# Kernel optimization log

Hardware: AMD Instinct MI355X
Metric: run time of the kernel (lower is better)

The kernel has to match this reference:

```python
import jax, jax.numpy as jnp
import numpy as np

B, N, DI, DS, DP, DM, S = 64, 4096, 64, 64, 64, 128, 7
NUM_ITER = 3
EPS_ATTN = 1e-8
LN_EPS = 1e-5


def setup_inputs() -> dict:
    key = jax.random.key(0)
    ks = jax.random.split(key, 12)
    rn = lambda k, shp, sc=1.0: (jax.random.normal(k, shp, jnp.float32) * sc)
    return {
        "x": rn(ks[0], (B, N, DI)),
        "ln_inp_g": jnp.ones((DI,), jnp.float32),
        "ln_inp_b": jnp.zeros((DI,), jnp.float32),
        "ln_slot_g": jnp.ones((DS,), jnp.float32),
        "ln_slot_b": jnp.zeros((DS,), jnp.float32),
        "slots_init": rn(ks[1], (1, S, DS)),
        "Wk": rn(ks[2], (DI, DP), 1.0 / np.sqrt(DI)),
        "Wv": rn(ks[3], (DI, DP), 1.0 / np.sqrt(DI)),
        "Wq": rn(ks[4], (DS, DP), 1.0 / np.sqrt(DS)),
        "gru_wih": rn(ks[5], (3 * DS, DP), 1.0 / np.sqrt(DS)),
        "gru_whh": rn(ks[6], (3 * DS, DS), 1.0 / np.sqrt(DS)),
        "gru_bih": jnp.zeros((3 * DS,), jnp.float32),
        "gru_bhh": jnp.zeros((3 * DS,), jnp.float32),
        "mlp_w1": rn(ks[7], (DS, DM), 1.0 / np.sqrt(DS)),
        "mlp_b1": jnp.zeros((DM,), jnp.float32),
        "mlp_w2": rn(ks[8], (DM, DS), 1.0 / np.sqrt(DM)),
        "mlp_b2": jnp.zeros((DS,), jnp.float32),
    }


def _layernorm(x, g, b):
    m = jnp.mean(x, axis=-1, keepdims=True)
    v = jnp.mean(jnp.square(x - m), axis=-1, keepdims=True)
    return (x - m) * jax.lax.rsqrt(v + LN_EPS) * g + b


def _gru_cell(u, h, wih, whh, bih, bhh):
    # PyTorch GRUCell semantics
    gi = u @ wih.T + bih  # [*, 3*DS]
    gh = h @ whh.T + bhh
    ir, iz, inn = jnp.split(gi, 3, axis=-1)
    hr, hz, hn = jnp.split(gh, 3, axis=-1)
    r = jax.nn.sigmoid(ir + hr)
    z = jax.nn.sigmoid(iz + hz)
    n = jnp.tanh(inn + r * hn)
    return (1.0 - z) * n + z * h


def reference(x, ln_inp_g, ln_inp_b, ln_slot_g, ln_slot_b, slots_init,
              Wk, Wv, Wq, gru_wih, gru_whh, gru_bih, gru_bhh,
              mlp_w1, mlp_b1, mlp_w2, mlp_b2):
    x = _layernorm(x, ln_inp_g, ln_inp_b)          # [B,N,DI]
    k = x @ Wk                                      # [B,N,DP] (hoisted; x fixed across iters)
    v = x @ Wv                                      # [B,N,DP]
    slots = jnp.broadcast_to(slots_init, (x.shape[0], S, DS))
    scale = 1.0 / np.sqrt(DP)
    for _ in range(NUM_ITER):
        slots_prev = slots
        sn = _layernorm(slots, ln_slot_g, ln_slot_b)
        q = sn @ Wq                                 # [B,S,DP]
        attn = jnp.einsum('bnd,bsd->bns', k, q) * scale
        attn = jax.nn.softmax(attn, axis=-1) + EPS_ATTN      # softmax over slots
        weights = attn / jnp.sum(attn, axis=1, keepdims=True)  # normalize over N
        updates = jnp.einsum('bns,bnd->bsd', weights, v)     # [B,S,DP]
        h = _gru_cell(updates.reshape(-1, DP), slots_prev.reshape(-1, DS),
                      gru_wih, gru_whh, gru_bih, gru_bhh)
        slots = h.reshape(-1, S, DS)
        slots = slots + (jax.nn.relu(slots @ mlp_w1 + mlp_b1) @ mlp_w2 + mlp_b2)
    return slots
```

## Files before the change

### kernel.cpp

```cpp
#include <hip/hip_runtime.h>
#include <stdint.h>

#define L2E 1.44269504088896f

static __device__ __forceinline__ float wsum(float v) {
    #pragma unroll
    for (int m = 1; m < 64; m <<= 1) v += __shfl_xor(v, m, 64);
    return v;
}
static __device__ __forceinline__ float sigm(float x) {
    return 1.0f / (1.0f + __builtin_amdgcn_exp2f(-x * L2E));
}
static __device__ __forceinline__ float tanh_(float x) {
    const float ax = fabsf(x);
    const float t = __builtin_amdgcn_exp2f(-2.0f * ax * L2E);
    const float r = (1.0f - t) / (1.0f + t);
    return (x < 0.f) ? -r : r;
}

template <int CTRL>
static __device__ __forceinline__ float dppterm(float v) {
    return __int_as_float(__builtin_amdgcn_update_dpp(
        0, __float_as_int(v), CTRL, 0xF, 0xF, true));
}
static __device__ __forceinline__ float red8(float v) {
    v += dppterm<0xB1>(v);
    v += dppterm<0x4E>(v);
    v += dppterm<0x141>(v);
    return v;
}

__global__ __launch_bounds__(256) void init_kernel(
    const float* __restrict__ s0,
    const float* __restrict__ lsg, const float* __restrict__ lsb,
    const float* __restrict__ Wq,  const float* __restrict__ Wk,
    const float* __restrict__ lig, const float* __restrict__ lib,
    const float* __restrict__ wih, const float* __restrict__ whh,
    float* __restrict__ slots, float* __restrict__ gkq, float* __restrict__ aux,
    float* __restrict__ wihT, float* __restrict__ whhT, float* __restrict__ WkT)
{
    __shared__ float wkT[4096];
    __shared__ float scr[4][64];
    const int tid = threadIdx.x, lane = tid & 63, wv = tid >> 6;
    const int idx = blockIdx.x * 256 + tid;

    if (idx < 12288) {
        const int i = idx / 192, j = idx - i * 192;
        wihT[idx] = wih[j * 64 + i];
    } else if (idx < 24576) {
        const int o = idx - 12288;
        const int i = o / 192, j = o - i * 192;
        whhT[o] = whh[j * 64 + i];
    } else {
        const int o = idx - 24576;
        const int p = o >> 6, d = o & 63;
        WkT[o] = Wk[d * 64 + p];
    }

    const int r = blockIdx.x * 4 + wv;
    const int s = r % 7;
    #pragma unroll
    for (int i = tid; i < 4096; i += 256) {
        const int d = i >> 6, p = i & 63;
        wkT[p * 64 + d] = Wk[i];
    }
    const float h = s0[s * 64 + lane];
    slots[r * 64 + lane] = h;
    __syncthreads();

    const float mean = wsum(h) * (1.0f / 64.0f);
    const float d = h - mean;
    const float var = wsum(d * d) * (1.0f / 64.0f);
    const float rs = rsqrtf(var + 1e-5f);
    const float sn = d * rs * lsg[lane] + lsb[lane];
    scr[wv][lane] = sn;
    __syncthreads();
    float q = 0.f;
    #pragma unroll 8
    for (int i = 0; i < 64; ++i) q = fmaf(scr[wv][i], Wq[i * 64 + lane], q);
    q *= 0.125f;
    __syncthreads();
    scr[wv][lane] = q;
    __syncthreads();
    float kq = 0.f;
    #pragma unroll 8
    for (int p = 0; p < 64; ++p) kq = fmaf(wkT[p * 64 + lane], scr[wv][p], kq);
    const float bk = wsum(lib[lane] * kq);
    const float gk = lig[lane] * kq;
    const float g1 = wsum(gk);
    gkq[r * 64 + lane] = gk;
    if (lane == 0) { aux[r * 2] = g1; aux[r * 2 + 1] = bk; }
}

__global__ __launch_bounds__(256, 2) void attn_kernel(
    const float* __restrict__ x,
    const float* __restrict__ gkq, const float* __restrict__ aux,
    float* __restrict__ Ypart)
{
    __shared__ float ybuf[16][460];
    const int tid = threadIdx.x, lane = tid & 63, wv = tid >> 6;
    const int b = blockIdx.x >> 4, chunk16 = blockIdx.x & 15;
    const int ck  = lane & 7;
    const int rsl = lane >> 3;

    float gk[7][8];
    {
        const float4* gp = (const float4*)(gkq + b * 448 + ck * 8);
        #pragma unroll
        for (int s = 0; s < 7; ++s) {
            const float4 u0 = gp[s * 16], u1 = gp[s * 16 + 1];
            gk[s][0] = u0.x; gk[s][1] = u0.y; gk[s][2] = u0.z; gk[s][3] = u0.w;
            gk[s][4] = u1.x; gk[s][5] = u1.y; gk[s][6] = u1.z; gk[s][7] = u1.w;
        }
    }
    const float* ab = aux + b * 14;
    float g1[7], bk[7];
    #pragma unroll
    for (int s = 0; s < 7; ++s) { g1[s] = ab[2 * s]; bk[s] = ab[2 * s + 1]; }

    float Yacc[7][8];
    #pragma unroll
    for (int s = 0; s < 7; ++s)
        #pragma unroll
        for (int j = 0; j < 8; ++j) Yacc[s][j] = 0.f;
    float cacc[7] = {0.f, 0.f, 0.f, 0.f, 0.f, 0.f, 0.f};

    const float* rb = x + (((long)b * 4096) + chunk16 * 256 + wv * 64 + rsl) * 64
                        + ck * 8;
    float4 a0 = *(const float4*)(rb);
    float4 a1 = *(const float4*)(rb + 4);
    #pragma unroll 1
    for (int g = 0; g < 8; ++g) {
        const int gn = (g < 7) ? g + 1 : 7;
        const float4 b0 = *(const float4*)(rb + gn * 512);
        const float4 b1 = *(const float4*)(rb + gn * 512 + 4);

        const float xv[8] = {a0.x, a0.y, a0.z, a0.w, a1.x, a1.y, a1.z, a1.w};
        float sum = 0.f, ss = 0.f;
        #pragma unroll
        for (int j = 0; j < 8; ++j) { sum += xv[j]; ss = fmaf(xv[j], xv[j], ss); }
        float acc[7];
        #pragma unroll
        for (int s = 0; s < 7; ++s) {
            float a = 0.f;
            #pragma unroll
            for (int j = 0; j < 8; ++j) a = fmaf(xv[j], gk[s][j], a);
            acc[s] = a;
        }
        sum = red8(sum);
        ss  = red8(ss);
        #pragma unroll
        for (int s = 0; s < 7; ++s) acc[s] = red8(acc[s]);

        const float m   = sum * (1.0f / 64.0f);
        const float var = ss * (1.0f / 64.0f) - m * m;
        const float rs  = rsqrtf(var + 1e-5f);
        const float rsm = rs * m;
        float t[7];
        #pragma unroll
        for (int s = 0; s < 7; ++s)
            t[s] = fmaf(rs, acc[s], fmaf(-rsm, g1[s], bk[s]));
        float mx = t[0];
        #pragma unroll
        for (int s = 1; s < 7; ++s) mx = fmaxf(mx, t[s]);
        float e[7], se = 0.f;
        #pragma unroll
        for (int s = 0; s < 7; ++s) {
            e[s] = __builtin_amdgcn_exp2f((t[s] - mx) * L2E);
            se += e[s];
        }
        const float inv = 1.0f / se;
        #pragma unroll
        for (int s = 0; s < 7; ++s) {
            const float w = fmaf(e[s], inv, 1e-8f);
            cacc[s] += w;
            const float wrs = w * rs;
            #pragma unroll
            for (int j = 0; j < 8; ++j)
                Yacc[s][j] = fmaf(wrs, xv[j], Yacc[s][j]);
        }
        a0 = b0; a1 = b1;
    }

    #pragma unroll
    for (int s = 0; s < 7; ++s) {
        #pragma unroll
        for (int j = 0; j < 8; ++j)
            Yacc[s][j] += dppterm<0x128>(Yacc[s][j]);
        cacc[s] += dppterm<0x128>(cacc[s]);
    }
    if (((lane >> 3) & 1) == 0) {
        const int sub = lane >> 4;
        float* yb = &ybuf[wv * 4 + sub][ck * 8];
        #pragma unroll
        for (int s = 0; s < 7; ++s) {
            #pragma unroll
            for (int j = 0; j < 8; ++j) yb[s * 64 + j] = Yacc[s][j];
        }
        if (ck == 0) {
            #pragma unroll
            for (int s = 0; s < 7; ++s)
                ybuf[wv * 4 + sub][448 + s] = cacc[s];
        }
    }
    __syncthreads();
    for (int i = tid; i < 455; i += 256) {
        float v = 0.f;
        #pragma unroll
        for (int p = 0; p < 16; ++p) v += ybuf[p][i];
        Ypart[((long)b * 16 + chunk16) * 456 + i] = v;
    }
}

__global__ __launch_bounds__(256) void update_kernel(
    const float* __restrict__ Ypart, float* __restrict__ slots,
    const float* __restrict__ Wv,
    const float* __restrict__ wihT, const float* __restrict__ whhT,
    const float* __restrict__ bih,  const float* __restrict__ bhh,
    const float* __restrict__ w1,   const float* __restrict__ b1,
    const float* __restrict__ w2,   const float* __restrict__ b2,
    const float* __restrict__ lsg,  const float* __restrict__ lsb,
    const float* __restrict__ Wq,   const float* __restrict__ WkT,
    const float* __restrict__ lig,  const float* __restrict__ lib,
    float* __restrict__ gkq, float* __restrict__ aux,
    float* __restrict__ out, int last)
{
    __shared__ float red[4][64];
    __shared__ float c16[16];
    __shared__ float ash[64];
    __shared__ float ush[64];
    __shared__ float hsh[64];
    __shared__ float gish[192], ghsh[192];
    __shared__ float hnsh[64];
    __shared__ float mbsh[128];
    __shared__ float qsh[64];
    const int tid = threadIdx.x, lane = tid & 63, wv = tid >> 6;
    const int r = blockIdx.x;
    const int b = r / 7, s = r - b * 7;
    const float* Yb = Ypart + (long)b * 16 * 456;

    float yp = 0.f;
    #pragma unroll
    for (int c = 0; c < 4; ++c)
        yp += Yb[(wv * 4 + c) * 456 + s * 64 + lane];
    red[wv][lane] = yp;
    if (tid < 16) c16[tid] = Yb[tid * 456 + 448 + s];
    if (tid >= 64 && tid < 128) hsh[tid - 64] = slots[r * 64 + (tid - 64)];
    __syncthreads();

    if (tid < 64) {
        const float Yd = red[0][lane] + red[1][lane] + red[2][lane] + red[3][lane];
        float C = 0.f;
        #pragma unroll
        for (int c = 0; c < 16; ++c) C += c16[c];
        const float Z = wsum(Yd) * (1.0f / 64.0f);
        ash[lane] = (lig[lane] * (Yd - Z) + lib[lane] * C) / C;
    }
    __syncthreads();

    float up = 0.f;
    #pragma unroll
    for (int i = 0; i < 16; ++i) {
        const int ii = wv * 16 + i;
        up = fmaf(ash[ii], Wv[ii * 64 + lane], up);
    }
    red[wv][lane] = up;
    __syncthreads();
    if (tid < 64) ush[lane] = red[0][lane] + red[1][lane] + red[2][lane] + red[3][lane];
    __syncthreads();

    if (tid < 192) {
        float a1 = bih[tid], a2 = bhh[tid];
        #pragma unroll 8
        for (int i = 0; i < 64; ++i) {
            a1 = fmaf(ush[i], wihT[i * 192 + tid], a1);
            a2 = fmaf(hsh[i], whhT[i * 192 + tid], a2);
        }
        gish[tid] = a1; ghsh[tid] = a2;
    }
    __syncthreads();
    if (tid < 64) {
        const float rr = sigm(gish[tid] + ghsh[tid]);
        const float zz = sigm(gish[64 + tid] + ghsh[64 + tid]);
        const float nn = tanh_(gish[128 + tid] + rr * ghsh[128 + tid]);
        hnsh[tid] = (1.f - zz) * nn + zz * hsh[tid];
    }
    __syncthreads();

    if (tid < 128) {
        float m = b1[tid];
        #pragma unroll 8
        for (int i = 0; i < 64; ++i) m = fmaf(hnsh[i], w1[i * 128 + tid], m);
        mbsh[tid] = fmaxf(m, 0.f);
    }
    __syncthreads();

    if (tid < 64) {
        float o = b2[tid];
        #pragma unroll 8
        for (int t = 0; t < 128; ++t) o = fmaf(mbsh[t], w2[t * 64 + tid], o);
        const float snv = hnsh[tid] + o;
        slots[r * 64 + tid] = snv;
        if (last) {
            out[r * 64 + tid] = snv;
        } else {
            const float mean = wsum(snv) * (1.0f / 64.0f);
            const float d = snv - mean;
            const float var = wsum(d * d) * (1.0f / 64.0f);
            const float rs = rsqrtf(var + 1e-5f);
            const float sn = d * rs * lsg[tid] + lsb[tid];
            ash[tid] = sn;
            float q = 0.f;
            #pragma unroll 8
            for (int i = 0; i < 64; ++i) q = fmaf(ash[i], Wq[i * 64 + tid], q);
            qsh[tid] = q * 0.125f;
            float kq = 0.f;
            #pragma unroll 8
            for (int p = 0; p < 64; ++p) kq = fmaf(WkT[p * 64 + tid], qsh[p], kq);
            const float bk = wsum(lib[tid] * kq);
            const float gk = lig[tid] * kq;
            const float g1 = wsum(gk);
            gkq[r * 64 + tid] = gk;
            if (tid == 0) { aux[r * 2] = g1; aux[r * 2 + 1] = bk; }
        }
    }
}

extern "C" void kernel_launch(void* const* d_in, const int* in_sizes, int n_in,
                              void* d_out, int out_size, void* d_ws, size_t ws_size,
                              hipStream_t stream)
{
    const float* x   = (const float*)d_in[0];
    const float* lig = (const float*)d_in[1];
    const float* lib = (const float*)d_in[2];
    const float* lsg = (const float*)d_in[3];
    const float* lsb = (const float*)d_in[4];
    const float* s0  = (const float*)d_in[5];
    const float* Wk  = (const float*)d_in[6];
    const float* Wv  = (const float*)d_in[7];
    const float* Wq  = (const float*)d_in[8];
    const float* wih = (const float*)d_in[9];
    const float* whh = (const float*)d_in[10];
    const float* bih = (const float*)d_in[11];
    const float* bhh = (const float*)d_in[12];
    const float* w1  = (const float*)d_in[13];
    const float* b1  = (const float*)d_in[14];
    const float* w2  = (const float*)d_in[15];
    const float* b2  = (const float*)d_in[16];

    float* f = (float*)d_ws;
    float* gkq   = f; f += 448 * 64;
    float* aux   = f; f += 448 * 2;
    float* slots = f; f += 448 * 64;
    float* Ypart = f; f += (long)64 * 16 * 456;
    float* wihT  = f; f += 64 * 192;
    float* whhT  = f; f += 64 * 192;
    float* WkT   = f; f += 64 * 64;

    init_kernel<<<112, 256, 0, stream>>>(s0, lsg, lsb, Wq, Wk, lig, lib,
                                         wih, whh, slots, gkq, aux,
                                         wihT, whhT, WkT);
    for (int it = 0; it < 3; ++it) {
        attn_kernel<<<1024, 256, 0, stream>>>(x, gkq, aux, Ypart);
        update_kernel<<<448, 256, 0, stream>>>(
            Ypart, slots, Wv, wihT, whhT, bih, bhh, w1, b1, w2, b2,
            lsg, lsb, Wq, WkT, lig, lib, gkq, aux,
            (float*)d_out, it == 2);
    }
}
```

Before: 227.8 us.

## Fuse attention and slot-update kernels with last-block-done atomic counter

Merges the per-iteration attention pass and the GRU/MLP slot update into one kernel. Each of the 16 chunk blocks per batch bumps an atomic counter, and the last one to finish reduces the partial sums and runs the update for all 7 slots, one wave per slot. This removes a kernel launch and the gap between kernels each iteration. It also software-pipelines the x loads two rows ahead. In exchange, the update work is serialized onto one block per batch with fewer threads per slot, plus threadfence and atomic overhead.

New measurement: 672.6 us. 2.95x slower.

```diff
diff --git a/kernel.cpp b/kernel.cpp
--- a/kernel.cpp
+++ b/kernel.cpp
@@ -37,12 +37,15 @@
     const float* __restrict__ lig, const float* __restrict__ lib,
     const float* __restrict__ wih, const float* __restrict__ whh,
     float* __restrict__ slots, float* __restrict__ gkq, float* __restrict__ aux,
-    float* __restrict__ wihT, float* __restrict__ whhT, float* __restrict__ WkT)
+    float* __restrict__ wihT, float* __restrict__ whhT, float* __restrict__ WkT,
+    int* __restrict__ cnt)
 {
     __shared__ float wkT[4096];
     __shared__ float scr[4][64];
     const int tid = threadIdx.x, lane = tid & 63, wv = tid >> 6;
     const int idx = blockIdx.x * 256 + tid;
+
+    if (idx < 192) cnt[idx] = 0;
 
     if (idx < 12288) {
         const int i = idx / 192, j = idx - i * 192;
@@ -92,128 +95,10 @@
     if (lane == 0) { aux[r * 2] = g1; aux[r * 2 + 1] = bk; }
 }
 
-__global__ __launch_bounds__(256, 2) void attn_kernel(
+__global__ __launch_bounds__(256, 2) void iter_kernel(
     const float* __restrict__ x,
-    const float* __restrict__ gkq, const float* __restrict__ aux,
-    float* __restrict__ Ypart)
-{
-    __shared__ float ybuf[16][460];
-    const int tid = threadIdx.x, lane = tid & 63, wv = tid >> 6;
-    const int b = blockIdx.x >> 4, chunk16 = blockIdx.x & 15;
-    const int ck  = lane & 7;
-    const int rsl = lane >> 3;
-
-    float gk[7][8];
-    {
-        const float4* gp = (const float4*)(gkq + b * 448 + ck * 8);
-        #pragma unroll
-        for (int s = 0; s < 7; ++s) {
-            const float4 u0 = gp[s * 16], u1 = gp[s * 16 + 1];
-            gk[s][0] = u0.x; gk[s][1] = u0.y; gk[s][2] = u0.z; gk[s][3] = u0.w;
-            gk[s][4] = u1.x; gk[s][5] = u1.y; gk[s][6] = u1.z; gk[s][7] = u1.w;
-        }
-    }
-    const float* ab = aux + b * 14;
-    float g1[7], bk[7];
-    #pragma unroll
-    for (int s = 0; s < 7; ++s) { g1[s] = ab[2 * s]; bk[s] = ab[2 * s + 1]; }
-
-    float Yacc[7][8];
-    #pragma unroll
-    for (int s = 0; s < 7; ++s)
-        #pragma unroll
-        for (int j = 0; j < 8; ++j) Yacc[s][j] = 0.f;
-    float cacc[7] = {0.f, 0.f, 0.f, 0.f, 0.f, 0.f, 0.f};
-
-    const float* rb = x + (((long)b * 4096) + chunk16 * 256 + wv * 64 + rsl) * 64
-                        + ck * 8;
-    float4 a0 = *(const float4*)(rb);
-    float4 a1 = *(const float4*)(rb + 4);
-    #pragma unroll 1
-    for (int g = 0; g < 8; ++g) {
-        const int gn = (g < 7) ? g + 1 : 7;
-        const float4 b0 = *(const float4*)(rb + gn * 512);
-        const float4 b1 = *(const float4*)(rb + gn * 512 + 4);
-
-        const float xv[8] = {a0.x, a0.y, a0.z, a0.w, a1.x, a1.y, a1.z, a1.w};
-        float sum = 0.f, ss = 0.f;
-        #pragma unroll
-        for (int j = 0; j < 8; ++j) { sum += xv[j]; ss = fmaf(xv[j], xv[j], ss); }
-        float acc[7];
-        #pragma unroll
-        for (int s = 0; s < 7; ++s) {
-            float a = 0.f;
-            #pragma unroll
-            for (int j = 0; j < 8; ++j) a = fmaf(xv[j], gk[s][j], a);
-            acc[s] = a;
-        }
-        sum = red8(sum);
-        ss  = red8(ss);
-        #pragma unroll
-        for (int s = 0; s < 7; ++s) acc[s] = red8(acc[s]);
-
-        const float m   = sum * (1.0f / 64.0f);
-        const float var = ss * (1.0f / 64.0f) - m * m;
-        const float rs  = rsqrtf(var + 1e-5f);
-        const float rsm = rs * m;
-        float t[7];
-        #pragma unroll
-        for (int s = 0; s < 7; ++s)
-            t[s] = fmaf(rs, acc[s], fmaf(-rsm, g1[s], bk[s]));
-        float mx = t[0];
-        #pragma unroll
-        for (int s = 1; s < 7; ++s) mx = fmaxf(mx, t[s]);
-        float e[7], se = 0.f;
-        #pragma unroll
-        for (int s = 0; s < 7; ++s) {
-            e[s] = __builtin_amdgcn_exp2f((t[s] - mx) * L2E);
-            se += e[s];
-        }
-        const float inv = 1.0f / se;
-        #pragma unroll
-        for (int s = 0; s < 7; ++s) {
-            const float w = fmaf(e[s], inv, 1e-8f);
-            cacc[s] += w;
-            const float wrs = w * rs;
-            #pragma unroll
-            for (int j = 0; j < 8; ++j)
-                Yacc[s][j] = fmaf(wrs, xv[j], Yacc[s][j]);
-        }
-        a0 = b0; a1 = b1;
-    }
-
-    #pragma unroll
-    for (int s = 0; s < 7; ++s) {
-        #pragma unroll
-        for (int j = 0; j < 8; ++j)
-            Yacc[s][j] += dppterm<0x128>(Yacc[s][j]);
-        cacc[s] += dppterm<0x128>(cacc[s]);
-    }
-    if (((lane >> 3) & 1) == 0) {
-        const int sub = lane >> 4;
-        float* yb = &ybuf[wv * 4 + sub][ck * 8];
-        #pragma unroll
-        for (int s = 0; s < 7; ++s) {
-            #pragma unroll
-            for (int j = 0; j < 8; ++j) yb[s * 64 + j] = Yacc[s][j];
-        }
-        if (ck == 0) {
-            #pragma unroll
-            for (int s = 0; s < 7; ++s)
-                ybuf[wv * 4 + sub][448 + s] = cacc[s];
-        }
-    }
-    __syncthreads();
-    for (int i = tid; i < 455; i += 256) {
-        float v = 0.f;
-        #pragma unroll
-        for (int p = 0; p < 16; ++p) v += ybuf[p][i];
-        Ypart[((long)b * 16 + chunk16) * 456 + i] = v;
-    }
-}
-
-__global__ __launch_bounds__(256) void update_kernel(
-    const float* __restrict__ Ypart, float* __restrict__ slots,
+    float* __restrict__ gkq, float* __restrict__ aux,
+    float* __restrict__ Ypart, float* __restrict__ slots,
     const float* __restrict__ Wv,
     const float* __restrict__ wihT, const float* __restrict__ whhT,
     const float* __restrict__ bih,  const float* __restrict__ bhh,
@@ -222,106 +107,241 @@
     const float* __restrict__ lsg,  const float* __restrict__ lsb,
     const float* __restrict__ Wq,   const float* __restrict__ WkT,
     const float* __restrict__ lig,  const float* __restrict__ lib,
-    float* __restrict__ gkq, float* __restrict__ aux,
-    float* __restrict__ out, int last)
+    int* __restrict__ cnt, float* __restrict__ out, int last)
 {
-    __shared__ float red[4][64];
-    __shared__ float c16[16];
-    __shared__ float ash[64];
-    __shared__ float ush[64];
-    __shared__ float hsh[64];
-    __shared__ float gish[192], ghsh[192];
-    __shared__ float hnsh[64];
-    __shared__ float mbsh[128];
-    __shared__ float qsh[64];
+    __shared__ float ybuf[16][460];
+    __shared__ float wsYd[7][64];
+    __shared__ float wsC[8];
+    __shared__ float wss[4][4][64];
+    __shared__ int lflag;
     const int tid = threadIdx.x, lane = tid & 63, wv = tid >> 6;
-    const int r = blockIdx.x;
-    const int b = r / 7, s = r - b * 7;
+    const int b = blockIdx.x >> 4, chunk16 = blockIdx.x & 15;
+    const int ck  = lane & 7;
+    const int rsl = lane >> 3;
+
+    float gk[7][8];
+    {
+        const float4* gp = (const float4*)(gkq + b * 448 + ck * 8);
+        #pragma unroll
+        for (int s = 0; s < 7; ++s) {
+            const float4 u0 = gp[s * 16], u1 = gp[s * 16 + 1];
+            gk[s][0] = u0.x; gk[s][1] = u0.y; gk[s][2] = u0.z; gk[s][3] = u0.w;
+            gk[s][4] = u1.x; gk[s][5] = u1.y; gk[s][6] = u1.z; gk[s][7] = u1.w;
+        }
+    }
+    const float* ab = aux + b * 14;
+    float g1[7], bk[7];
+    #pragma unroll
+    for (int s = 0; s < 7; ++s) { g1[s] = ab[2 * s]; bk[s] = ab[2 * s + 1]; }
+
+    float Yacc[7][8];
+    #pragma unroll
+    for (int s = 0; s < 7; ++s)
+        #pragma unroll
+        for (int j = 0; j < 8; ++j) Yacc[s][j] = 0.f;
+    float cacc[7] = {0.f, 0.f, 0.f, 0.f, 0.f, 0.f, 0.f};
+
+    const float* rb = x + (((long)b * 4096) + chunk16 * 256 + wv * 64 + rsl) * 64
+                        + ck * 8;
+
+    auto process = [&](const float4& u0, const float4& u1) {
+        const float xv[8] = {u0.x, u0.y, u0.z, u0.w, u1.x, u1.y, u1.z, u1.w};
+        float sum = 0.f, ss = 0.f;
+        #pragma unroll
+        for (int j = 0; j < 8; ++j) { sum += xv[j]; ss = fmaf(xv[j], xv[j], ss); }
+        float acc[7];
+        #pragma unroll
+        for (int s = 0; s < 7; ++s) {
+            float a = 0.f;
+            #pragma unroll
+            for (int j = 0; j < 8; ++j) a = fmaf(xv[j], gk[s][j], a);
+            acc[s] = a;
+        }
+        sum = red8(sum);
+        ss  = red8(ss);
+        #pragma unroll
+        for (int s = 0; s < 7; ++s) acc[s] = red8(acc[s]);
+
+        const float m   = sum * (1.0f / 64.0f);
+        const float var = ss * (1.0f / 64.0f) - m * m;
+        const float rs  = rsqrtf(var + 1e-5f);
+        const float rsm = rs * m;
+        float t[7];
+        #pragma unroll
+        for (int s = 0; s < 7; ++s)
+            t[s] = fmaf(rs, acc[s], fmaf(-rsm, g1[s], bk[s]));
+        float mx = t[0];
+        #pragma unroll
+        for (int s = 1; s < 7; ++s) mx = fmaxf(mx, t[s]);
+        float e[7], se = 0.f;
+        #pragma unroll
+        for (int s = 0; s < 7; ++s) {
+            e[s] = __builtin_amdgcn_exp2f((t[s] - mx) * L2E);
+            se += e[s];
+        }
+        const float inv = 1.0f / se;
+        #pragma unroll
+        for (int s = 0; s < 7; ++s) {
+            const float w = fmaf(e[s], inv, 1e-8f);
+            cacc[s] += w;
+            const float wrs = w * rs;
+            #pragma unroll
+            for (int j = 0; j < 8; ++j)
+                Yacc[s][j] = fmaf(wrs, xv[j], Yacc[s][j]);
+        }
+    };
+
+    float4 pa0 = *(const float4*)(rb);
+    float4 pa1 = *(const float4*)(rb + 4);
+    float4 pb0 = *(const float4*)(rb + 512);
+    float4 pb1 = *(const float4*)(rb + 516);
+    #pragma unroll 1
+    for (int g = 0; g < 8; g += 2) {
+        const int g2 = (g + 2 < 8) ? g + 2 : 6;
+        const int g3 = (g + 3 < 8) ? g + 3 : 7;
+        const float4 na0 = *(const float4*)(rb + g2 * 512);
+        const float4 na1 = *(const float4*)(rb + g2 * 512 + 4);
+        process(pa0, pa1);
+        const float4 nb0 = *(const float4*)(rb + g3 * 512);
+        const float4 nb1 = *(const float4*)(rb + g3 * 512 + 4);
+        process(pb0, pb1);
+        pa0 = na0; pa1 = na1; pb0 = nb0; pb1 = nb1;
+    }
+
+    #pragma unroll
+    for (int s = 0; s < 7; ++s) {
+        #pragma unroll
+        for (int j = 0; j < 8; ++j)
+            Yacc[s][j] += dppterm<0x128>(Yacc[s][j]);
+        cacc[s] += dppterm<0x128>(cacc[s]);
+    }
+    if (((lane >> 3) & 1) == 0) {
+        const int sub = lane >> 4;
+        float* yb = &ybuf[wv * 4 + sub][ck * 8];
+        #pragma unroll
+        for (int s = 0; s < 7; ++s) {
+            #pragma unroll
+            for (int j = 0; j < 8; ++j) yb[s * 64 + j] = Yacc[s][j];
+        }
+        if (ck == 0) {
+            #pragma unroll
+            for (int s = 0; s < 7; ++s)
+                ybuf[wv * 4 + sub][448 + s] = cacc[s];
+        }
+    }
+    __syncthreads();
+    for (int i = tid; i < 455; i += 256) {
+        float v = 0.f;
+        #pragma unroll
+        for (int p = 0; p < 16; ++p) v += ybuf[p][i];
+        Ypart[((long)b * 16 + chunk16) * 456 + i] = v;
+    }
+
+    __threadfence();
+    __syncthreads();
+    if (tid == 0) {
+        const int old = atomicAdd(&cnt[b], 1);
+        lflag = (old == 15) ? 1 : 0;
+    }
+    __syncthreads();
+    if (!lflag) return;
+    __threadfence();
+
     const float* Yb = Ypart + (long)b * 16 * 456;
-
-    float yp = 0.f;
-    #pragma unroll
-    for (int c = 0; c < 4; ++c)
-        yp += Yb[(wv * 4 + c) * 456 + s * 64 + lane];
-    red[wv][lane] = yp;
-    if (tid < 16) c16[tid] = Yb[tid * 456 + 448 + s];
-    if (tid >= 64 && tid < 128) hsh[tid - 64] = slots[r * 64 + (tid - 64)];
-    __syncthreads();
-
-    if (tid < 64) {
-        const float Yd = red[0][lane] + red[1][lane] + red[2][lane] + red[3][lane];
-        float C = 0.f;
-        #pragma unroll
-        for (int c = 0; c < 16; ++c) C += c16[c];
-        const float Z = wsum(Yd) * (1.0f / 64.0f);
-        ash[lane] = (lig[lane] * (Yd - Z) + lib[lane] * C) / C;
-    }
-    __syncthreads();
-
-    float up = 0.f;
-    #pragma unroll
-    for (int i = 0; i < 16; ++i) {
-        const int ii = wv * 16 + i;
-        up = fmaf(ash[ii], Wv[ii * 64 + lane], up);
-    }
-    red[wv][lane] = up;
-    __syncthreads();
-    if (tid < 64) ush[lane] = red[0][lane] + red[1][lane] + red[2][lane] + red[3][lane];
-    __syncthreads();
-
-    if (tid < 192) {
-        float a1 = bih[tid], a2 = bhh[tid];
+    for (int o = tid; o < 448; o += 256) {
+        float v = 0.f;
+        #pragma unroll
+        for (int c = 0; c < 16; ++c) v += Yb[c * 456 + o];
+        wsYd[o >> 6][o & 63] = v;
+    }
+    if (tid < 7) {
+        float v = 0.f;
+        #pragma unroll
+        for (int c = 0; c < 16; ++c) v += Yb[c * 456 + 448 + tid];
+        wsC[tid] = v;
+    }
+    __syncthreads();
+
+    float (*scr)[64] = wss[wv];
+    #pragma unroll 1
+    for (int sp = 0; sp < 2; ++sp) {
+        const int s = wv + sp * 4;
+        if (s >= 7) break;
+        const int r = b * 7 + s;
+
+        const float Yd = wsYd[s][lane];
+        const float C  = wsC[s];
+        const float Z  = wsum(Yd) * (1.0f / 64.0f);
+        const float a  = (lig[lane] * (Yd - Z) + lib[lane] * C) / C;
+        scr[0][lane] = a;
+        float u = 0.f;
+        #pragma unroll 8
+        for (int i = 0; i < 64; ++i) u = fmaf(scr[0][i], Wv[i * 64 + lane], u);
+        const float h = slots[r * 64 + lane];
+        scr[1][lane] = u;
+        scr[2][lane] = h;
+
+        float gi0 = bih[lane], gi1 = bih[64 + lane], gi2 = bih[128 + lane];
+        float gh0 = bhh[lane], gh1 = bhh[64 + lane], gh2 = bhh[128 + lane];
+        #pragma unroll 4
+        for (int i = 0; i < 64; ++i) {
+            const float ui = scr[1][i], hi = scr[2][i];
+            const float* wi = &wihT[i * 192];
+            const float* wh = &whhT[i * 192];
+            gi0 = fmaf(ui, wi[lane], gi0);
+            gi1 = fmaf(ui, wi[64 + lane], gi1);
+            gi2 = fmaf(ui, wi[128 + lane], gi2);
+            gh0 = fmaf(hi, wh[lane], gh0);
+            gh1 = fmaf(hi, wh[64 + lane], gh1);
+            gh2 = fmaf(hi, wh[128 + lane], gh2);
+        }
+        const float rr = sigm(gi0 + gh0);
+        const float zz = sigm(gi1 + gh1);
+        const float nn = tanh_(gi2 + rr * gh2);
+        const float hn = (1.f - zz) * nn + zz * h;
+        scr[0][lane] = hn;
+
+        float m0 = b1[lane], m1 = b1[64 + lane];
         #pragma unroll 8
         for (int i = 0; i < 64; ++i) {
-            a1 = fmaf(ush[i], wihT[i * 192 + tid], a1);
-            a2 = fmaf(hsh[i], whhT[i * 192 + tid], a2);
-        }
-        gish[tid] = a1; ghsh[tid] = a2;
-    }
-    __syncthreads();
-    if (tid < 64) {
-        const float rr = sigm(gish[tid] + ghsh[tid]);
-        const float zz = sigm(gish[64 + tid] + ghsh[64 + tid]);
-        const float nn = tanh_(gish[128 + tid] + rr * ghsh[128 + tid]);
-        hnsh[tid] = (1.f - zz) * nn + zz * hsh[tid];
-    }
-    __syncthreads();
-
-    if (tid < 128) {
-        float m = b1[tid];
+            const float hi = scr[0][i];
+            m0 = fmaf(hi, w1[i * 128 + lane], m0);
+            m1 = fmaf(hi, w1[i * 128 + 64 + lane], m1);
+        }
+        scr[1][lane] = fmaxf(m0, 0.f);
+        scr[2][lane] = fmaxf(m1, 0.f);
+
+        float o2 = b2[lane];
         #pragma unroll 8
-        for (int i = 0; i < 64; ++i) m = fmaf(hnsh[i], w1[i * 128 + tid], m);
-        mbsh[tid] = fmaxf(m, 0.f);
-    }
-    __syncthreads();
-
-    if (tid < 64) {
-        float o = b2[tid];
+        for (int t = 0; t < 64; ++t)
+            o2 = fmaf(scr[1][t], w2[t * 64 + lane], o2);
         #pragma unroll 8
-        for (int t = 0; t < 128; ++t) o = fmaf(mbsh[t], w2[t * 64 + tid], o);
-        const float snv = hnsh[tid] + o;
-        slots[r * 64 + tid] = snv;
+        for (int t = 0; t < 64; ++t)
+            o2 = fmaf(scr[2][t], w2[(64 + t) * 64 + lane], o2);
+        const float snv = hn + o2;
+        slots[r * 64 + lane] = snv;
         if (last) {
-            out[r * 64 + tid] = snv;
+            out[r * 64 + lane] = snv;
         } else {
             const float mean = wsum(snv) * (1.0f / 64.0f);
             const float d = snv - mean;
             const float var = wsum(d * d) * (1.0f / 64.0f);
             const float rs = rsqrtf(var + 1e-5f);
-            const float sn = d * rs * lsg[tid] + lsb[tid];
-            ash[tid] = sn;
+            const float sn = d * rs * lsg[lane] + lsb[lane];
+            scr[3][lane] = sn;
             float q = 0.f;
             #pragma unroll 8
-            for (int i = 0; i < 64; ++i) q = fmaf(ash[i], Wq[i * 64 + tid], q);
-            qsh[tid] = q * 0.125f;
+            for (int i = 0; i < 64; ++i) q = fmaf(scr[3][i], Wq[i * 64 + lane], q);
+            q *= 0.125f;
+            scr[0][lane] = q;
             float kq = 0.f;
             #pragma unroll 8
-            for (int p = 0; p < 64; ++p) kq = fmaf(WkT[p * 64 + tid], qsh[p], kq);
-            const float bk = wsum(lib[tid] * kq);
-            const float gk = lig[tid] * kq;
-            const float g1 = wsum(gk);
-            gkq[r * 64 + tid] = gk;
-            if (tid == 0) { aux[r * 2] = g1; aux[r * 2 + 1] = bk; }
+            for (int p = 0; p < 64; ++p) kq = fmaf(WkT[p * 64 + lane], scr[0][p], kq);
+            const float bk2 = wsum(lib[lane] * kq);
+            const float gkv = lig[lane] * kq;
+            const float g1v = wsum(gkv);
+            gkq[r * 64 + lane] = gkv;
+            if (lane == 0) { aux[r * 2] = g1v; aux[r * 2 + 1] = bk2; }
         }
     }
 }
@@ -356,15 +376,15 @@
     float* wihT  = f; f += 64 * 192;
     float* whhT  = f; f += 64 * 192;
     float* WkT   = f; f += 64 * 64;
+    int*   cnt   = (int*)f;  f += 192;
 
     init_kernel<<<112, 256, 0, stream>>>(s0, lsg, lsb, Wq, Wk, lig, lib,
                                          wih, whh, slots, gkq, aux,
-                                         wihT, whhT, WkT);
+                                         wihT, whhT, WkT, cnt);
     for (int it = 0; it < 3; ++it) {
-        attn_kernel<<<1024, 256, 0, stream>>>(x, gkq, aux, Ypart);
-        update_kernel<<<448, 256, 0, stream>>>(
-            Ypart, slots, Wv, wihT, whhT, bih, bhh, w1, b1, w2, b2,
-            lsg, lsb, Wq, WkT, lig, lib, gkq, aux,
-            (float*)d_out, it == 2);
-    }
-}
+        iter_kernel<<<1024, 256, 0, stream>>>(
+            x, gkq, aux, Ypart, slots, Wv, wihT, whhT, bih, bhh,
+            w1, b1, w2, b2, lsg, lsb, Wq, WkT, lig, lib,
+            cnt + it * 64, (float*)d_out, it == 2);
+    }
+}
```

## Spread each attention row across 16 lanes to cut registers and raise occupancy

Applied to the files above, without the earlier changes.

The attention kernel now maps each 64-wide input row onto 16 lanes holding float4 each, where before it used 8 lanes holding 8 floats. This halves the per-thread gk and Yacc register arrays, allowing launch bounds of 4 blocks per CU instead of 2. Each cross-lane reduction gains one DPP step (red16) and the loop runs 16 iterations instead of 8, but the final DPP merge and lane-masked store disappear, and shared-memory writes become float4. The intent is more waves to hide global memory latency, paid for with extra reduction instructions per row.

Measured after the change: 245.3 us. 7.7% more time.

```diff
diff --git a/kernel.cpp b/kernel.cpp
--- a/kernel.cpp
+++ b/kernel.cpp
@@ -23,10 +23,11 @@
     return __int_as_float(__builtin_amdgcn_update_dpp(
         0, __float_as_int(v), CTRL, 0xF, 0xF, true));
 }
-static __device__ __forceinline__ float red8(float v) {
+static __device__ __forceinline__ float red16(float v) {
     v += dppterm<0xB1>(v);
     v += dppterm<0x4E>(v);
-    v += dppterm<0x141>(v);
+    v += dppterm<0x124>(v);
+    v += dppterm<0x128>(v);
     return v;
 }
 
@@ -92,7 +93,7 @@
     if (lane == 0) { aux[r * 2] = g1; aux[r * 2 + 1] = bk; }
 }
 
-__global__ __launch_bounds__(256, 2) void attn_kernel(
+__global__ __launch_bounds__(256, 4) void attn_kernel(
     const float* __restrict__ x,
     const float* __restrict__ gkq, const float* __restrict__ aux,
     float* __restrict__ Ypart)
@@ -100,17 +101,16 @@
     __shared__ float ybuf[16][460];
     const int tid = threadIdx.x, lane = tid & 63, wv = tid >> 6;
     const int b = blockIdx.x >> 4, chunk16 = blockIdx.x & 15;
-    const int ck  = lane & 7;
-    const int rsl = lane >> 3;
-
-    float gk[7][8];
+    const int ck  = lane & 15;
+    const int rsl = lane >> 4;
+
+    float gk[7][4];
     {
-        const float4* gp = (const float4*)(gkq + b * 448 + ck * 8);
-        #pragma unroll
-        for (int s = 0; s < 7; ++s) {
-            const float4 u0 = gp[s * 16], u1 = gp[s * 16 + 1];
-            gk[s][0] = u0.x; gk[s][1] = u0.y; gk[s][2] = u0.z; gk[s][3] = u0.w;
-            gk[s][4] = u1.x; gk[s][5] = u1.y; gk[s][6] = u1.z; gk[s][7] = u1.w;
+        const float4* gp = (const float4*)(gkq + b * 448 + ck * 4);
+        #pragma unroll
+        for (int s = 0; s < 7; ++s) {
+            const float4 u = gp[s * 16];
+            gk[s][0] = u.x; gk[s][1] = u.y; gk[s][2] = u.z; gk[s][3] = u.w;
         }
     }
     const float* ab = aux + b * 14;
@@ -118,39 +118,38 @@
     #pragma unroll
     for (int s = 0; s < 7; ++s) { g1[s] = ab[2 * s]; bk[s] = ab[2 * s + 1]; }
 
-    float Yacc[7][8];
+    float Yacc[7][4];
     #pragma unroll
     for (int s = 0; s < 7; ++s)
         #pragma unroll
-        for (int j = 0; j < 8; ++j) Yacc[s][j] = 0.f;
+        for (int j = 0; j < 4; ++j) Yacc[s][j] = 0.f;
     float cacc[7] = {0.f, 0.f, 0.f, 0.f, 0.f, 0.f, 0.f};
 
     const float* rb = x + (((long)b * 4096) + chunk16 * 256 + wv * 64 + rsl) * 64
-                        + ck * 8;
-    float4 a0 = *(const float4*)(rb);
-    float4 a1 = *(const float4*)(rb + 4);
+                        + ck * 4;
+    float4 cur = *(const float4*)(rb);
     #pragma unroll 1
-    for (int g = 0; g < 8; ++g) {
-        const int gn = (g < 7) ? g + 1 : 7;
-        const float4 b0 = *(const float4*)(rb + gn * 512);
-        const float4 b1 = *(const float4*)(rb + gn * 512 + 4);
-
-        const float xv[8] = {a0.x, a0.y, a0.z, a0.w, a1.x, a1.y, a1.z, a1.w};
-        float sum = 0.f, ss = 0.f;
-        #pragma unroll
-        for (int j = 0; j < 8; ++j) { sum += xv[j]; ss = fmaf(xv[j], xv[j], ss); }
+    for (int g = 0; g < 16; ++g) {
+        const int gn = (g < 15) ? g + 1 : 15;
+        const float4 nxt = *(const float4*)(rb + gn * 256);
+
+        const float xv[4] = {cur.x, cur.y, cur.z, cur.w};
+        float sum = (xv[0] + xv[1]) + (xv[2] + xv[3]);
+        float ss = 0.f;
+        #pragma unroll
+        for (int j = 0; j < 4; ++j) ss = fmaf(xv[j], xv[j], ss);
         float acc[7];
         #pragma unroll
         for (int s = 0; s < 7; ++s) {
             float a = 0.f;
             #pragma unroll
-            for (int j = 0; j < 8; ++j) a = fmaf(xv[j], gk[s][j], a);
+            for (int j = 0; j < 4; ++j) a = fmaf(xv[j], gk[s][j], a);
             acc[s] = a;
         }
-        sum = red8(sum);
-        ss  = red8(ss);
-        #pragma unroll
-        for (int s = 0; s < 7; ++s) acc[s] = red8(acc[s]);
+        sum = red16(sum);
+        ss  = red16(ss);
+        #pragma unroll
+        for (int s = 0; s < 7; ++s) acc[s] = red16(acc[s]);
 
         const float m   = sum * (1.0f / 64.0f);
         const float var = ss * (1.0f / 64.0f) - m * m;
@@ -176,31 +175,25 @@
             cacc[s] += w;
             const float wrs = w * rs;
             #pragma unroll
-            for (int j = 0; j < 8; ++j)
+            for (int j = 0; j < 4; ++j)
                 Yacc[s][j] = fmaf(wrs, xv[j], Yacc[s][j]);
         }
-        a0 = b0; a1 = b1;
-    }
-
-    #pragma unroll
-    for (int s = 0; s < 7; ++s) {
-        #pragma unroll
-        for (int j = 0; j < 8; ++j)
-            Yacc[s][j] += dppterm<0x128>(Yacc[s][j]);
-        cacc[s] += dppterm<0x128>(cacc[s]);
-    }
-    if (((lane >> 3) & 1) == 0) {
-        const int sub = lane >> 4;
-        float* yb = &ybuf[wv * 4 + sub][ck * 8];
-        #pragma unroll
-        for (int s = 0; s < 7; ++s) {
-            #pragma unroll
-            for (int j = 0; j < 8; ++j) yb[s * 64 + j] = Yacc[s][j];
+        cur = nxt;
+    }
+
+    {
+        float* yb = &ybuf[wv * 4 + rsl][0];
+        #pragma unroll
+        for (int s = 0; s < 7; ++s) {
+            float4 o;
+            o.x = Yacc[s][0]; o.y = Yacc[s][1];
+            o.z = Yacc[s][2]; o.w = Yacc[s][3];
+            *(float4*)&yb[s * 64 + ck * 4] = o;
         }
         if (ck == 0) {
             #pragma unroll
-            for (int s = 0; s < 7; ++s)
-                ybuf[wv * 4 + sub][448 + s] = cacc[s];
+            for (int s = 0; s < 7; ++s) yb[448 + s] = cacc[s];
+            yb[455] = 0.f;
         }
     }
     __syncthreads();
```
